# Kernel optimization log

Hardware: AMD Instinct MI355X
Metric: run time of the kernel (lower is better)

The kernel has to match this reference:

```python
import jax, jax.numpy as jnp
import numpy as np

EPS = 1e-5
DIM = 1024

def layer_norm(x, gamma, beta):
    mu = jnp.mean(x, axis=-1, keepdims=True)
    var = jnp.var(x, axis=-1, keepdims=True)
    return (x - mu) * jax.lax.rsqrt(var + EPS) * gamma + beta

def setup_inputs() -> dict:
    key = jax.random.key(0)
    k1, k2 = jax.random.split(key)
    return {
        "image_features": jax.random.normal(k1, (32, 1024, DIM), dtype=jnp.float32),
        "text_features": jax.random.normal(k2, (32, 512, DIM), dtype=jnp.float32),
        "gamma": jnp.ones((DIM,), dtype=jnp.float32),
        "beta": jnp.zeros((DIM,), dtype=jnp.float32),
    }

def reference(image_features, text_features, gamma, beta):
    scale = DIM ** (-0.5)
    image_norm = layer_norm(image_features, gamma, beta)   # [B, Ni, D]
    text_norm = layer_norm(text_features, gamma, beta)     # [B, Nt, D]
    # shared attention matrix, softmax only over text axis
    attn = jax.nn.softmax(jnp.einsum('bid,btd->bit', image_norm, text_norm) * scale, axis=-1)  # [B, Ni, Nt]
    image_attended = jnp.einsum('bit,btd->bid', attn, text_norm)   # [B, Ni, D]
    text_attended = jnp.einsum('bit,bid->btd', attn, image_norm)   # [B, Nt, D] (attn reused transposed, no re-softmax)
    return (image_features + image_attended, text_features + text_attended)
```

## Files before the change

### kernel.cpp

```cpp
#include <hip/hip_runtime.h>
#include <hip/hip_bf16.h>

#define B_  32
#define NI_ 1024
#define NT_ 512
#define D_  1024

typedef __attribute__((ext_vector_type(8))) short bf16x8;
typedef __attribute__((ext_vector_type(4))) float f32x4;

__device__ __forceinline__ ushort f2b(float f) {
  unsigned u = __builtin_bit_cast(unsigned, f);
  u = (u + 0x7FFFu + ((u >> 16) & 1u)) >> 16;
  return (ushort)u;
}


__global__ __launch_bounds__(256) void ln_bf16_kernel(
    const float* __restrict__ x, const float* __restrict__ gamma,
    const float* __restrict__ beta, ushort* __restrict__ out)
{
  const int row  = blockIdx.x * 4 + (threadIdx.x >> 6);
  const int lane = threadIdx.x & 63;
  const float* xr = x + (size_t)row * D_;
  float4 v[4];
  float s = 0.f, sq = 0.f;
#pragma unroll
  for (int q = 0; q < 4; ++q) {
    v[q] = *reinterpret_cast<const float4*>(xr + q * 256 + lane * 4);
    s  += v[q].x + v[q].y + v[q].z + v[q].w;
    sq += v[q].x*v[q].x + v[q].y*v[q].y + v[q].z*v[q].z + v[q].w*v[q].w;
  }
#pragma unroll
  for (int m = 1; m < 64; m <<= 1) {
    s  += __shfl_xor(s,  m);
    sq += __shfl_xor(sq, m);
  }
  const float mean = s * (1.f / D_);
  const float rstd = rsqrtf(sq * (1.f / D_) - mean * mean + 1e-5f);
  ushort* orow = out + (size_t)row * D_;
#pragma unroll
  for (int q = 0; q < 4; ++q) {
    const float4 g  = *reinterpret_cast<const float4*>(gamma + q * 256 + lane * 4);
    const float4 bt = *reinterpret_cast<const float4*>(beta  + q * 256 + lane * 4);
    ushort4 o;
    o.x = f2b((v[q].x - mean) * rstd * g.x + bt.x);
    o.y = f2b((v[q].y - mean) * rstd * g.y + bt.y);
    o.z = f2b((v[q].z - mean) * rstd * g.z + bt.z);
    o.w = f2b((v[q].w - mean) * rstd * g.w + bt.w);
    *reinterpret_cast<ushort4*>(orow + q * 256 + lane * 4) = o;
  }
}

__global__ __launch_bounds__(256) void transpose_bf16_kernel(
    const ushort* __restrict__ in, ushort* __restrict__ out, int R, int C)
{
  __shared__ ushort lds[64][68];
  const size_t nb = (size_t)blockIdx.z * (size_t)R * C;
  const ushort* ib = in + nb;
  ushort* ob = out + nb;
  const int c0 = blockIdx.x * 64, r0 = blockIdx.y * 64;
  const int t = threadIdx.x;
#pragma unroll
  for (int it = 0; it < 2; ++it) {
    const int r = (t >> 3) + 32 * it;
    const int c = (t & 7) * 8;
    uint4 val = *reinterpret_cast<const uint4*>(ib + (size_t)(r0 + r) * C + c0 + c);
    *reinterpret_cast<uint2*>(&lds[r][c])     = make_uint2(val.x, val.y);
    *reinterpret_cast<uint2*>(&lds[r][c + 4]) = make_uint2(val.z, val.w);
  }
  __syncthreads();
#pragma unroll
  for (int it = 0; it < 2; ++it) {
    const int c  = (t >> 3) + 32 * it;
    const int rb = (t & 7) * 8;
    union { ushort u[8]; uint4 v; } pk;
#pragma unroll
    for (int j = 0; j < 8; ++j) pk.u[j] = lds[rb + j][c];
    *reinterpret_cast<uint4*>(ob + (size_t)(c0 + c) * R + r0 + rb) = pk.v;
  }
}

__global__ __launch_bounds__(512) void qk_softmax_kernel(
    const ushort* __restrict__ qn,
    const ushort* __restrict__ kn,
    ushort* __restrict__ attn_it,
    ushort* __restrict__ attn_ti)
{
  __shared__ __align__(16) ushort Asm[2][64 * 32];
  __shared__ __align__(16) ushort Bsm[2][512 * 32];
  __shared__ __align__(16) float redm[64][8];
  __shared__ __align__(16) float reds[64][8];

  const int bid = blockIdx.x;
  const int sid = (bid & 7) * 64 + (bid >> 3);
  const int b   = sid >> 4;
  const int i0  = (sid & 15) * 64;
  const int tid  = threadIdx.x;
  const int w    = tid >> 6;
  const int lane = tid & 63;
  const int lr   = lane & 15;
  const int g    = lane >> 4;

  const ushort* qb = qn + ((size_t)b * NI_ + i0) * D_;
  const ushort* kb = kn + (size_t)b * NT_ * D_;

  const int srow = tid >> 2;
  const int scol = (tid & 3) * 8;
  const int wp = (((tid >> 6) << 6) | (((tid >> 2) & 15) << 2)
                | ((tid & 3) ^ ((tid >> 3) & 3))) * 8;
  const int chunkLane = ((lane & 15) << 2) | ((lane >> 4) ^ ((lane >> 1) & 3));

  uint4 ra, rb0, rb1, rb2, rb3;
  auto LOAD = [&](int t) {
    const int ko = t * 32 + scol;
    if (tid < 256) ra = *reinterpret_cast<const uint4*>(qb + (size_t)srow * D_ + ko);
    rb0 = *reinterpret_cast<const uint4*>(kb + (size_t)(srow      ) * D_ + ko);
    rb1 = *reinterpret_cast<const uint4*>(kb + (size_t)(srow + 128) * D_ + ko);
    rb2 = *reinterpret_cast<const uint4*>(kb + (size_t)(srow + 256) * D_ + ko);
    rb3 = *reinterpret_cast<const uint4*>(kb + (size_t)(srow + 384) * D_ + ko);
  };
  auto WRITE = [&](int nb) {
    if (tid < 256) *reinterpret_cast<uint4*>(&Asm[nb][wp]) = ra;
    *reinterpret_cast<uint4*>(&Bsm[nb][wp        ]) = rb0;
    *reinterpret_cast<uint4*>(&Bsm[nb][wp +  4096]) = rb1;
    *reinterpret_cast<uint4*>(&Bsm[nb][wp +  8192]) = rb2;
    *reinterpret_cast<uint4*>(&Bsm[nb][wp + 12288]) = rb3;
  };

  f32x4 acc[4][4];
#pragma unroll
  for (int i = 0; i < 4; ++i)
#pragma unroll
    for (int j = 0; j < 4; ++j) acc[i][j] = (f32x4){0.f, 0.f, 0.f, 0.f};

  LOAD(0); WRITE(0); __syncthreads();
  const int nst = D_ / 32;
  int cur = 0;
  for (int t = 0; t < nst; ++t) {
    if (t + 1 < nst) LOAD(t + 1);
    const ushort* As = Asm[cur];
    const ushort* Bs = Bsm[cur];
    bf16x8 af[4], bf[4];
#pragma unroll
    for (int i = 0; i < 4; ++i)
      af[i] = *reinterpret_cast<const bf16x8*>(As + (i * 64 + chunkLane) * 8);
#pragma unroll
    for (int j = 0; j < 4; ++j)
      bf[j] = *reinterpret_cast<const bf16x8*>(Bs + ((w * 4 + j) * 64 + chunkLane) * 8);
#pragma unroll
    for (int i = 0; i < 4; ++i)
#pragma unroll
      for (int j = 0; j < 4; ++j)
        acc[i][j] = __builtin_amdgcn_mfma_f32_16x16x32_bf16(af[i], bf[j], acc[i][j], 0, 0, 0);
    __syncthreads();
    if (t + 1 < nst) WRITE(cur ^ 1);
    __syncthreads();
    cur ^= 1;
  }

  const float c1 = 0.03125f * 1.44269504f;

  float mx[4][4];
#pragma unroll
  for (int i = 0; i < 4; ++i)
#pragma unroll
    for (int r = 0; r < 4; ++r) {
      float m = fmaxf(fmaxf(acc[i][0][r], acc[i][1][r]),
                      fmaxf(acc[i][2][r], acc[i][3][r]));
      m = fmaxf(m, __shfl_xor(m, 1));
      m = fmaxf(m, __shfl_xor(m, 2));
      m = fmaxf(m, __shfl_xor(m, 4));
      m = fmaxf(m, __shfl_xor(m, 8));
      mx[i][r] = m;
    }
  if (lr == 0) {
#pragma unroll
    for (int i = 0; i < 4; ++i)
#pragma unroll
      for (int r = 0; r < 4; ++r) redm[i * 16 + g * 4 + r][w] = mx[i][r];
  }
  __syncthreads();
  float gm[4][4];
#pragma unroll
  for (int i = 0; i < 4; ++i)
#pragma unroll
    for (int r = 0; r < 4; ++r) {
      const int row = i * 16 + g * 4 + r;
      const float4 a0 = *reinterpret_cast<const float4*>(&redm[row][0]);
      const float4 a1 = *reinterpret_cast<const float4*>(&redm[row][4]);
      gm[i][r] = fmaxf(fmaxf(fmaxf(a0.x, a0.y), fmaxf(a0.z, a0.w)),
                       fmaxf(fmaxf(a1.x, a1.y), fmaxf(a1.z, a1.w)));
    }

  float sm[4][4];
#pragma unroll
  for (int i = 0; i < 4; ++i)
#pragma unroll
    for (int r = 0; r < 4; ++r) sm[i][r] = 0.f;
#pragma unroll
  for (int i = 0; i < 4; ++i)
#pragma unroll
    for (int j = 0; j < 4; ++j)
#pragma unroll
      for (int r = 0; r < 4; ++r) {
        const float p = exp2f((acc[i][j][r] - gm[i][r]) * c1);
        acc[i][j][r] = p;
        sm[i][r] += p;
      }
#pragma unroll
  for (int i = 0; i < 4; ++i)
#pragma unroll
    for (int r = 0; r < 4; ++r) {
      float s = sm[i][r];
      s += __shfl_xor(s, 1);
      s += __shfl_xor(s, 2);
      s += __shfl_xor(s, 4);
      s += __shfl_xor(s, 8);
      sm[i][r] = s;
    }
  if (lr == 0) {
#pragma unroll
    for (int i = 0; i < 4; ++i)
#pragma unroll
      for (int r = 0; r < 4; ++r) reds[i * 16 + g * 4 + r][w] = sm[i][r];
  }
  __syncthreads();
  float inv[4][4];
#pragma unroll
  for (int i = 0; i < 4; ++i)
#pragma unroll
    for (int r = 0; r < 4; ++r) {
      const int row = i * 16 + g * 4 + r;
      const float4 a0 = *reinterpret_cast<const float4*>(&reds[row][0]);
      const float4 a1 = *reinterpret_cast<const float4*>(&reds[row][4]);
      inv[i][r] = 1.f / (a0.x + a0.y + a0.z + a0.w + a1.x + a1.y + a1.z + a1.w);
    }

#pragma unroll
  for (int i = 0; i < 4; ++i) {
    const int rbase = i0 + i * 16 + g * 4;
#pragma unroll
    for (int j = 0; j < 4; ++j) {
      const int tcol = w * 64 + j * 16 + lr;
      ushort4 pk;
      pk.x = f2b(acc[i][j][0] * inv[i][0]);
      pk.y = f2b(acc[i][j][1] * inv[i][1]);
      pk.z = f2b(acc[i][j][2] * inv[i][2]);
      pk.w = f2b(acc[i][j][3] * inv[i][3]);
      ushort* it_p = attn_it + ((size_t)b * NI_ + rbase) * NT_ + tcol;
      it_p[0 * NT_] = pk.x;
      it_p[1 * NT_] = pk.y;
      it_p[2 * NT_] = pk.z;
      it_p[3 * NT_] = pk.w;
      *reinterpret_cast<ushort4*>(attn_ti + ((size_t)b * NT_ + tcol) * NI_ + rbase) = pk;
    }
  }
}

__global__ __launch_bounds__(256) void bt_gemm_add_kernel(
    const ushort* __restrict__ A,
    const ushort* __restrict__ Bm,
    const float* __restrict__ add,
    float* __restrict__ out,
    int M, int N, int K)
{
  __shared__ __align__(16) ushort Asm[2][128 * 32];
  __shared__ __align__(16) ushort Bsm[2][128 * 32];

  const int b    = blockIdx.z;
  const int m0   = blockIdx.y * 128;
  const int n0   = blockIdx.x * 128;
  const int tid  = threadIdx.x;
  const int w    = tid >> 6;
  const int lane = tid & 63;
  const int lr   = lane & 15;
  const int g    = lane >> 4;

  const ushort* Ab = A  + ((size_t)b * M + m0) * K;
  const ushort* Bb = Bm + ((size_t)b * N + n0) * K;

  const int srow = tid >> 2;
  const int scol = (tid & 3) * 8;
  const int wp = (((tid >> 6) << 6) | (((tid >> 2) & 15) << 2)
                | ((tid & 3) ^ ((tid >> 3) & 3))) * 8;
  const int chunkLane = ((lane & 15) << 2) | ((lane >> 4) ^ ((lane >> 1) & 3));

  uint4 ra0, ra1, rbx0, rbx1;
  auto LOAD = [&](int t) {
    const int ko = t * 32 + scol;
    ra0  = *reinterpret_cast<const uint4*>(Ab + (size_t)(srow     ) * K + ko);
    ra1  = *reinterpret_cast<const uint4*>(Ab + (size_t)(srow + 64) * K + ko);
    rbx0 = *reinterpret_cast<const uint4*>(Bb + (size_t)(srow     ) * K + ko);
    rbx1 = *reinterpret_cast<const uint4*>(Bb + (size_t)(srow + 64) * K + ko);
  };
  auto WRITE = [&](int nb) {
    *reinterpret_cast<uint4*>(&Asm[nb][wp       ]) = ra0;
    *reinterpret_cast<uint4*>(&Asm[nb][wp + 2048]) = ra1;
    *reinterpret_cast<uint4*>(&Bsm[nb][wp       ]) = rbx0;
    *reinterpret_cast<uint4*>(&Bsm[nb][wp + 2048]) = rbx1;
  };

  f32x4 acc[4][4];
#pragma unroll
  for (int i = 0; i < 4; ++i)
#pragma unroll
    for (int j = 0; j < 4; ++j) acc[i][j] = (f32x4){0.f, 0.f, 0.f, 0.f};

  LOAD(0); WRITE(0); __syncthreads();
  const int nst = K / 32;
  int cur = 0;
  for (int t = 0; t < nst; ++t) {
    if (t + 1 < nst) LOAD(t + 1);
    const ushort* As = Asm[cur];
    const ushort* Bs = Bsm[cur];
    bf16x8 af[4], bf[4];
#pragma unroll
    for (int i = 0; i < 4; ++i)
      af[i] = *reinterpret_cast<const bf16x8*>(
          As + (((w >> 1) * 4 + i) * 64 + chunkLane) * 8);
#pragma unroll
    for (int j = 0; j < 4; ++j)
      bf[j] = *reinterpret_cast<const bf16x8*>(
          Bs + (((w & 1) * 4 + j) * 64 + chunkLane) * 8);
#pragma unroll
    for (int i = 0; i < 4; ++i)
#pragma unroll
      for (int j = 0; j < 4; ++j)
        acc[i][j] = __builtin_amdgcn_mfma_f32_16x16x32_bf16(af[i], bf[j], acc[i][j], 0, 0, 0);
    __syncthreads();
    if (t + 1 < nst) WRITE(cur ^ 1);
    __syncthreads();
    cur ^= 1;
  }

  const size_t ob = (size_t)b * M * N;
  const int rbase = m0 + (w >> 1) * 64 + g * 4;
#pragma unroll
  for (int i = 0; i < 4; ++i)
#pragma unroll
    for (int j = 0; j < 4; ++j) {
      const int c = n0 + (w & 1) * 64 + j * 16 + lr;
#pragma unroll
      for (int r = 0; r < 4; ++r) {
        const size_t idx = ob + (size_t)(rbase + i * 16 + r) * N + c;
        out[idx] = add[idx] + acc[i][j][r];
      }
    }
}

extern "C" void kernel_launch(void* const* d_in, const int* in_sizes, int n_in,
                              void* d_out, int out_size, void* d_ws, size_t ws_size,
                              hipStream_t stream) {
  const float* imgf  = (const float*)d_in[0];
  const float* txtf  = (const float*)d_in[1];
  const float* gamma = (const float*)d_in[2];
  const float* beta  = (const float*)d_in[3];

  float* out0 = (float*)d_out;
  float* out1 = out0 + (size_t)B_ * NI_ * D_;

  const size_t SZ = (size_t)B_ * NT_ * NI_ * 2;
  char* ws = (char*)d_ws;
  ushort* attn_ti = (ushort*)ws;
  ushort* attn_it = (ushort*)(ws + SZ);
  ushort* txnT    = (ushort*)(ws + 2 * SZ);
  ushort* imnT    = (ushort*)(ws + SZ);
  ushort* imn     = (ushort*)out1;
  ushort* txn     = (ushort*)out0;

  ln_bf16_kernel<<<(B_ * NI_) / 4, 256, 0, stream>>>(imgf, gamma, beta, imn);
  ln_bf16_kernel<<<(B_ * NT_) / 4, 256, 0, stream>>>(txtf, gamma, beta, txn);
  qk_softmax_kernel<<<(NI_ / 64) * B_, 512, 0, stream>>>(imn, txn, attn_it, attn_ti);
  transpose_bf16_kernel<<<dim3(D_ / 64, NT_ / 64, B_), 256, 0, stream>>>(txn, txnT, NT_, D_);
  bt_gemm_add_kernel<<<dim3(D_ / 128, NI_ / 128, B_), 256, 0, stream>>>(
      attn_it, txnT, imgf, out0, NI_, D_, NT_);
  transpose_bf16_kernel<<<dim3(D_ / 64, NI_ / 64, B_), 256, 0, stream>>>(imn, imnT, NI_, D_);
  bt_gemm_add_kernel<<<dim3(D_ / 128, NT_ / 128, B_), 256, 0, stream>>>(
      attn_ti, imnT, txtf, out1, NT_, D_, NI_);
}
```

Before: 334.5 us.

## Use direct global-to-LDS loads with a four-stage pipeline in the output GEMM

The bt_gemm_add kernel now stages its A and B tiles through global_load_lds, which writes straight into shared memory without passing through registers. The LDS ring grows from two buffers to four and runs three tiles ahead, synchronised with explicit vmcnt waits and a single barrier per k-step instead of two. The aim is to hide global-load latency and drop the register round trip and one barrier. In exchange it uses more LDS, which may lower occupancy. The bank-conflict swizzle is removed in favour of a linear fragment layout, so LDS reads may conflict, and the race-freedom of the four-buffer reuse depends on the barrier ordering.

Result: slower. 364.2 us (+8.9%).

```diff
diff --git a/kernel.cpp b/kernel.cpp
--- a/kernel.cpp
+++ b/kernel.cpp
@@ -15,6 +15,13 @@
   return (ushort)u;
 }
 
+__device__ __forceinline__ void gll16(const ushort* g, ushort* l) {
+  __builtin_amdgcn_global_load_lds(
+      (const __attribute__((address_space(1))) void*)g,
+      (__attribute__((address_space(3))) void*)l, 16, 0, 0);
+}
+
+#define VMWAIT(N) asm volatile("s_waitcnt vmcnt(" #N ")" ::: "memory")
 
 __global__ __launch_bounds__(256) void ln_bf16_kernel(
     const float* __restrict__ x, const float* __restrict__ gamma,
@@ -265,8 +272,8 @@
     float* __restrict__ out,
     int M, int N, int K)
 {
-  __shared__ __align__(16) ushort Asm[2][128 * 32];
-  __shared__ __align__(16) ushort Bsm[2][128 * 32];
+  __shared__ __align__(16) ushort Asm[4][128 * 32];
+  __shared__ __align__(16) ushort Bsm[4][128 * 32];
 
   const int b    = blockIdx.z;
   const int m0   = blockIdx.y * 128;
@@ -280,26 +287,20 @@
   const ushort* Ab = A  + ((size_t)b * M + m0) * K;
   const ushort* Bb = Bm + ((size_t)b * N + n0) * K;
 
-  const int srow = tid >> 2;
-  const int scol = (tid & 3) * 8;
-  const int wp = (((tid >> 6) << 6) | (((tid >> 2) & 15) << 2)
-                | ((tid & 3) ^ ((tid >> 3) & 3))) * 8;
-  const int chunkLane = ((lane & 15) << 2) | ((lane >> 4) ^ ((lane >> 1) & 3));
-
-  uint4 ra0, ra1, rbx0, rbx1;
-  auto LOAD = [&](int t) {
-    const int ko = t * 32 + scol;
-    ra0  = *reinterpret_cast<const uint4*>(Ab + (size_t)(srow     ) * K + ko);
-    ra1  = *reinterpret_cast<const uint4*>(Ab + (size_t)(srow + 64) * K + ko);
-    rbx0 = *reinterpret_cast<const uint4*>(Bb + (size_t)(srow     ) * K + ko);
-    rbx1 = *reinterpret_cast<const uint4*>(Bb + (size_t)(srow + 64) * K + ko);
+  auto ISSUE = [&](int u) {
+    const int nb = u & 3;
+    const int ko = u * 32;
+#pragma unroll
+    for (int q = 0; q < 2; ++q) {
+      const int c   = q * 256 + tid;
+      const int row = ((c >> 6) << 4) | (c & 15);
+      const int kc  = (c >> 4) & 3;
+      const size_t go = (size_t)row * K + ko + kc * 8;
+      const int lbase = (q * 256 + w * 64) * 8;
+      gll16(Ab + go, &Asm[nb][lbase]);
+      gll16(Bb + go, &Bsm[nb][lbase]);
+    }
   };
-  auto WRITE = [&](int nb) {
-    *reinterpret_cast<uint4*>(&Asm[nb][wp       ]) = ra0;
-    *reinterpret_cast<uint4*>(&Asm[nb][wp + 2048]) = ra1;
-    *reinterpret_cast<uint4*>(&Bsm[nb][wp       ]) = rbx0;
-    *reinterpret_cast<uint4*>(&Bsm[nb][wp + 2048]) = rbx1;
-  };
 
   f32x4 acc[4][4];
 #pragma unroll
@@ -307,31 +308,35 @@
 #pragma unroll
     for (int j = 0; j < 4; ++j) acc[i][j] = (f32x4){0.f, 0.f, 0.f, 0.f};
 
-  LOAD(0); WRITE(0); __syncthreads();
   const int nst = K / 32;
-  int cur = 0;
+  ISSUE(0); ISSUE(1); ISSUE(2);
+
   for (int t = 0; t < nst; ++t) {
-    if (t + 1 < nst) LOAD(t + 1);
-    const ushort* As = Asm[cur];
-    const ushort* Bs = Bsm[cur];
+    if (t + 2 < nst)      VMWAIT(8);
+    else if (t + 1 < nst) VMWAIT(4);
+    else                  VMWAIT(0);
+    __builtin_amdgcn_sched_barrier(0);
+    __builtin_amdgcn_s_barrier();
+    __builtin_amdgcn_sched_barrier(0);
+
+    const ushort* As = Asm[t & 3];
+    const ushort* Bs = Bsm[t & 3];
     bf16x8 af[4], bf[4];
 #pragma unroll
     for (int i = 0; i < 4; ++i)
       af[i] = *reinterpret_cast<const bf16x8*>(
-          As + (((w >> 1) * 4 + i) * 64 + chunkLane) * 8);
+          As + (((w >> 1) * 4 + i) * 64 + lane) * 8);
 #pragma unroll
     for (int j = 0; j < 4; ++j)
       bf[j] = *reinterpret_cast<const bf16x8*>(
-          Bs + (((w & 1) * 4 + j) * 64 + chunkLane) * 8);
+          Bs + (((w & 1) * 4 + j) * 64 + lane) * 8);
 #pragma unroll
     for (int i = 0; i < 4; ++i)
 #pragma unroll
       for (int j = 0; j < 4; ++j)
         acc[i][j] = __builtin_amdgcn_mfma_f32_16x16x32_bf16(af[i], bf[j], acc[i][j], 0, 0, 0);
-    __syncthreads();
-    if (t + 1 < nst) WRITE(cur ^ 1);
-    __syncthreads();
-    cur ^= 1;
+
+    if (t + 3 < nst) ISSUE(t + 3);
   }
 
   const size_t ob = (size_t)b * M * N;
```

## Fuse attn·V GEMM and residual add into QK-softmax kernel

Applied to the files above, without the earlier changes.

The QK-softmax kernel now keeps its normalized 64x512 attention tile in shared memory and multiplies it directly by the transposed text features to produce image_attended plus the residual. This drops the separate image-side GEMM launch and the write and re-read of the attn_it matrix. In exchange, the fused kernel loads V operands straight from global memory with no LDS staging or double buffering, holds 128 more accumulator registers per thread, and makes uncoalesced scalar fp32 output stores, which may lower occupancy and efficiency. Workspace buffers are also reassigned so the normalized inputs no longer alias the output tensors.

Result: slower. 363.7 us (+8.7%).

```diff
diff --git a/kernel.cpp b/kernel.cpp
--- a/kernel.cpp
+++ b/kernel.cpp
@@ -14,7 +14,6 @@
   u = (u + 0x7FFFu + ((u >> 16) & 1u)) >> 16;
   return (ushort)u;
 }
-
 
 __global__ __launch_bounds__(256) void ln_bf16_kernel(
     const float* __restrict__ x, const float* __restrict__ gamma,
@@ -81,14 +80,15 @@
   }
 }
 
-__global__ __launch_bounds__(512) void qk_softmax_kernel(
+__global__ __launch_bounds__(512) void attn_fused_kernel(
     const ushort* __restrict__ qn,
     const ushort* __restrict__ kn,
-    ushort* __restrict__ attn_it,
-    ushort* __restrict__ attn_ti)
+    const ushort* __restrict__ vt,
+    const float*  __restrict__ addm,
+    ushort* __restrict__ attn_ti,
+    float*  __restrict__ out0)
 {
-  __shared__ __align__(16) ushort Asm[2][64 * 32];
-  __shared__ __align__(16) ushort Bsm[2][512 * 32];
+  __shared__ __align__(16) ushort raw[36864];
   __shared__ __align__(16) float redm[64][8];
   __shared__ __align__(16) float reds[64][8];
 
@@ -121,11 +121,13 @@
     rb3 = *reinterpret_cast<const uint4*>(kb + (size_t)(srow + 384) * D_ + ko);
   };
   auto WRITE = [&](int nb) {
-    if (tid < 256) *reinterpret_cast<uint4*>(&Asm[nb][wp]) = ra;
-    *reinterpret_cast<uint4*>(&Bsm[nb][wp        ]) = rb0;
-    *reinterpret_cast<uint4*>(&Bsm[nb][wp +  4096]) = rb1;
-    *reinterpret_cast<uint4*>(&Bsm[nb][wp +  8192]) = rb2;
-    *reinterpret_cast<uint4*>(&Bsm[nb][wp + 12288]) = rb3;
+    ushort* As = raw + nb * 2048;
+    ushort* Bs = raw + 4096 + nb * 16384;
+    if (tid < 256) *reinterpret_cast<uint4*>(&As[wp]) = ra;
+    *reinterpret_cast<uint4*>(&Bs[wp        ]) = rb0;
+    *reinterpret_cast<uint4*>(&Bs[wp +  4096]) = rb1;
+    *reinterpret_cast<uint4*>(&Bs[wp +  8192]) = rb2;
+    *reinterpret_cast<uint4*>(&Bs[wp + 12288]) = rb3;
   };
 
   f32x4 acc[4][4];
@@ -139,8 +141,8 @@
   int cur = 0;
   for (int t = 0; t < nst; ++t) {
     if (t + 1 < nst) LOAD(t + 1);
-    const ushort* As = Asm[cur];
-    const ushort* Bs = Bsm[cur];
+    const ushort* As = raw + cur * 2048;
+    const ushort* Bs = raw + 4096 + cur * 16384;
     bf16x8 af[4], bf[4];
 #pragma unroll
     for (int i = 0; i < 4; ++i)
@@ -237,6 +239,7 @@
       inv[i][r] = 1.f / (a0.x + a0.y + a0.z + a0.w + a1.x + a1.y + a1.z + a1.w);
     }
 
+  ushort* P = raw;
 #pragma unroll
   for (int i = 0; i < 4; ++i) {
     const int rbase = i0 + i * 16 + g * 4;
@@ -248,14 +251,53 @@
       pk.y = f2b(acc[i][j][1] * inv[i][1]);
       pk.z = f2b(acc[i][j][2] * inv[i][2]);
       pk.w = f2b(acc[i][j][3] * inv[i][3]);
-      ushort* it_p = attn_it + ((size_t)b * NI_ + rbase) * NT_ + tcol;
-      it_p[0 * NT_] = pk.x;
-      it_p[1 * NT_] = pk.y;
-      it_p[2 * NT_] = pk.z;
-      it_p[3 * NT_] = pk.w;
       *reinterpret_cast<ushort4*>(attn_ti + ((size_t)b * NT_ + tcol) * NI_ + rbase) = pk;
-    }
-  }
+      const int prow = i * 16 + g * 4;
+      P[(prow + 0) * 520 + tcol] = pk.x;
+      P[(prow + 1) * 520 + tcol] = pk.y;
+      P[(prow + 2) * 520 + tcol] = pk.z;
+      P[(prow + 3) * 520 + tcol] = pk.w;
+    }
+  }
+  __syncthreads();
+
+  f32x4 apv[4][8];
+#pragma unroll
+  for (int i = 0; i < 4; ++i)
+#pragma unroll
+    for (int n = 0; n < 8; ++n) apv[i][n] = (f32x4){0.f, 0.f, 0.f, 0.f};
+
+  const ushort* vb = vt + (size_t)b * D_ * NT_;
+#pragma unroll 1
+  for (int ts = 0; ts < NT_ / 32; ++ts) {
+    bf16x8 paf[4], pbf[8];
+#pragma unroll
+    for (int i = 0; i < 4; ++i)
+      paf[i] = *reinterpret_cast<const bf16x8*>(P + (i * 16 + lr) * 520 + ts * 32 + g * 8);
+#pragma unroll
+    for (int n = 0; n < 8; ++n)
+      pbf[n] = *reinterpret_cast<const bf16x8*>(
+          vb + (size_t)(w * 128 + n * 16 + lr) * NT_ + ts * 32 + g * 8);
+#pragma unroll
+    for (int i = 0; i < 4; ++i)
+#pragma unroll
+      for (int n = 0; n < 8; ++n)
+        apv[i][n] = __builtin_amdgcn_mfma_f32_16x16x32_bf16(paf[i], pbf[n], apv[i][n], 0, 0, 0);
+  }
+
+  const float* addb = addm + ((size_t)b * NI_ + i0) * D_;
+  float* outb = out0 + ((size_t)b * NI_ + i0) * D_;
+#pragma unroll
+  for (int i = 0; i < 4; ++i)
+#pragma unroll
+    for (int n = 0; n < 8; ++n) {
+      const int col = w * 128 + n * 16 + lr;
+#pragma unroll
+      for (int r = 0; r < 4; ++r) {
+        const int idx = (i * 16 + g * 4 + r) * D_ + col;
+        outb[idx] = addb[idx] + apv[i][n][r];
+      }
+    }
 }
 
 __global__ __launch_bounds__(256) void bt_gemm_add_kernel(
@@ -360,21 +402,19 @@
   float* out0 = (float*)d_out;
   float* out1 = out0 + (size_t)B_ * NI_ * D_;
 
-  const size_t SZ = (size_t)B_ * NT_ * NI_ * 2;
+  const size_t MB32 = (size_t)B_ * NT_ * NI_ * 2;
   char* ws = (char*)d_ws;
   ushort* attn_ti = (ushort*)ws;
-  ushort* attn_it = (ushort*)(ws + SZ);
-  ushort* txnT    = (ushort*)(ws + 2 * SZ);
-  ushort* imnT    = (ushort*)(ws + SZ);
-  ushort* imn     = (ushort*)out1;
-  ushort* txn     = (ushort*)out0;
+  ushort* txnT    = (ushort*)(ws +     MB32);
+  ushort* imnT    = (ushort*)(ws + 2 * MB32);
+  ushort* txn     = (ushort*)(ws + 4 * MB32);
+  ushort* imn     = (ushort*)(ws + 5 * MB32);
 
   ln_bf16_kernel<<<(B_ * NI_) / 4, 256, 0, stream>>>(imgf, gamma, beta, imn);
   ln_bf16_kernel<<<(B_ * NT_) / 4, 256, 0, stream>>>(txtf, gamma, beta, txn);
-  qk_softmax_kernel<<<(NI_ / 64) * B_, 512, 0, stream>>>(imn, txn, attn_it, attn_ti);
   transpose_bf16_kernel<<<dim3(D_ / 64, NT_ / 64, B_), 256, 0, stream>>>(txn, txnT, NT_, D_);
-  bt_gemm_add_kernel<<<dim3(D_ / 128, NI_ / 128, B_), 256, 0, stream>>>(
-      attn_it, txnT, imgf, out0, NI_, D_, NT_);
+  attn_fused_kernel<<<(NI_ / 64) * B_, 512, 0, stream>>>(
+      imn, txn, txnT, imgf, attn_ti, out0);
   transpose_bf16_kernel<<<dim3(D_ / 64, NI_ / 64, B_), 256, 0, stream>>>(imn, imnT, NI_, D_);
   bt_gemm_add_kernel<<<dim3(D_ / 128, NT_ / 128, B_), 256, 0, stream>>>(
       attn_ti, imnT, txtf, out1, NT_, D_, NI_);
```

## Store attention and transposed operands in MFMA-ready panel layout for GEMMs

Applied to the files above, without the earlier changes.

The softmax and transpose kernels now write their bf16 outputs directly into a tiled panel layout of 128-row by 32-k tiles, already in the MFMA fragment order. The GEMM kernel can then load each tile with fully contiguous 16-byte reads and copy it into LDS without swizzling or scattered strided row access. The cost is more scattered 2-byte and 8-byte stores in the softmax epilogue. Workspace usage also grows, because normalized inputs move from the output buffers into separate workspace regions, and the unswizzled LDS reads may hit bank conflicts.

Measured after the change: 359.2 us. +7.4%, slower.

```diff
diff --git a/kernel.cpp b/kernel.cpp
--- a/kernel.cpp
+++ b/kernel.cpp
@@ -52,15 +52,14 @@
   }
 }
 
-__global__ __launch_bounds__(256) void transpose_bf16_kernel(
-    const ushort* __restrict__ in, ushort* __restrict__ out, int R, int C)
+__global__ __launch_bounds__(256) void transpose_pan_kernel(
+    const ushort* __restrict__ in, ushort* __restrict__ outp, int R, int C)
 {
   __shared__ ushort lds[64][68];
-  const size_t nb = (size_t)blockIdx.z * (size_t)R * C;
-  const ushort* ib = in + nb;
-  ushort* ob = out + nb;
+  const ushort* ib = in + (size_t)blockIdx.z * (size_t)R * C;
   const int c0 = blockIdx.x * 64, r0 = blockIdx.y * 64;
   const int t = threadIdx.x;
+  const int nMT = C >> 7, nKS = R >> 5;
 #pragma unroll
   for (int it = 0; it < 2; ++it) {
     const int r = (t >> 3) + 32 * it;
@@ -77,15 +76,19 @@
     union { ushort u[8]; uint4 v; } pk;
 #pragma unroll
     for (int j = 0; j < 8; ++j) pk.u[j] = lds[rb + j][c];
-    *reinterpret_cast<uint4*>(ob + (size_t)(c0 + c) * R + r0 + rb) = pk.v;
+    const int n  = c0 + c;
+    const int kb = r0 + rb;
+    const size_t tb = ((size_t)blockIdx.z * nMT + (n >> 7)) * nKS + (kb >> 5);
+    const int ch = (((n & 127) >> 4) << 6) | (((kb >> 3) & 3) << 4) | (n & 15);
+    *reinterpret_cast<uint4*>(outp + tb * 4096 + ch * 8) = pk.v;
   }
 }
 
 __global__ __launch_bounds__(512) void qk_softmax_kernel(
     const ushort* __restrict__ qn,
     const ushort* __restrict__ kn,
-    ushort* __restrict__ attn_it,
-    ushort* __restrict__ attn_ti)
+    ushort* __restrict__ ap5,
+    ushort* __restrict__ ap7)
 {
   __shared__ __align__(16) ushort Asm[2][64 * 32];
   __shared__ __align__(16) ushort Bsm[2][512 * 32];
@@ -237,9 +240,14 @@
       inv[i][r] = 1.f / (a0.x + a0.y + a0.z + a0.w + a1.x + a1.y + a1.z + a1.w);
     }
 
+  const int mt5 = i0 >> 7;
 #pragma unroll
   for (int i = 0; i < 4; ++i) {
     const int rbase = i0 + i * 16 + g * 4;
+    const int R5hi  = ((i0 >> 6) & 1) * 4 + i;
+    const int ks7   = rbase >> 5;
+    const int kc7   = (rbase >> 3) & 3;
+    const int el7   = rbase & 7;
 #pragma unroll
     for (int j = 0; j < 4; ++j) {
       const int tcol = w * 64 + j * 16 + lr;
@@ -248,19 +256,23 @@
       pk.y = f2b(acc[i][j][1] * inv[i][1]);
       pk.z = f2b(acc[i][j][2] * inv[i][2]);
       pk.w = f2b(acc[i][j][3] * inv[i][3]);
-      ushort* it_p = attn_it + ((size_t)b * NI_ + rbase) * NT_ + tcol;
-      it_p[0 * NT_] = pk.x;
-      it_p[1 * NT_] = pk.y;
-      it_p[2 * NT_] = pk.z;
-      it_p[3 * NT_] = pk.w;
-      *reinterpret_cast<ushort4*>(attn_ti + ((size_t)b * NT_ + tcol) * NI_ + rbase) = pk;
+      const size_t tb7 = ((size_t)(b * 4 + (tcol >> 7)) * 32 + ks7) * 4096;
+      const int c7 = (((tcol & 127) >> 4) << 6) | (kc7 << 4) | lr;
+      *reinterpret_cast<ushort4*>(ap7 + tb7 + c7 * 8 + el7) = pk;
+      const size_t tb5 = ((size_t)(b * 8 + mt5) * 16 + (tcol >> 5)) * 4096;
+      const int c5 = (R5hi << 6) | (((tcol >> 3) & 3) << 4) | (g * 4);
+      ushort* p5 = ap5 + tb5 + (size_t)c5 * 8 + (tcol & 7);
+      p5[0]  = pk.x;
+      p5[8]  = pk.y;
+      p5[16] = pk.z;
+      p5[24] = pk.w;
     }
   }
 }
 
 __global__ __launch_bounds__(256) void bt_gemm_add_kernel(
-    const ushort* __restrict__ A,
-    const ushort* __restrict__ Bm,
+    const ushort* __restrict__ Apan,
+    const ushort* __restrict__ Bpan,
     const float* __restrict__ add,
     float* __restrict__ out,
     int M, int N, int K)
@@ -276,29 +288,25 @@
   const int lane = tid & 63;
   const int lr   = lane & 15;
   const int g    = lane >> 4;
-
-  const ushort* Ab = A  + ((size_t)b * M + m0) * K;
-  const ushort* Bb = Bm + ((size_t)b * N + n0) * K;
-
-  const int srow = tid >> 2;
-  const int scol = (tid & 3) * 8;
-  const int wp = (((tid >> 6) << 6) | (((tid >> 2) & 15) << 2)
-                | ((tid & 3) ^ ((tid >> 3) & 3))) * 8;
-  const int chunkLane = ((lane & 15) << 2) | ((lane >> 4) ^ ((lane >> 1) & 3));
+  const int nst  = K / 32;
+
+  const ushort* Ab = Apan + ((size_t)(b * (M >> 7) + (m0 >> 7)) * nst) * 4096;
+  const ushort* Bb = Bpan + ((size_t)(b * (N >> 7) + (n0 >> 7)) * nst) * 4096;
 
   uint4 ra0, ra1, rbx0, rbx1;
   auto LOAD = [&](int t) {
-    const int ko = t * 32 + scol;
-    ra0  = *reinterpret_cast<const uint4*>(Ab + (size_t)(srow     ) * K + ko);
-    ra1  = *reinterpret_cast<const uint4*>(Ab + (size_t)(srow + 64) * K + ko);
-    rbx0 = *reinterpret_cast<const uint4*>(Bb + (size_t)(srow     ) * K + ko);
-    rbx1 = *reinterpret_cast<const uint4*>(Bb + (size_t)(srow + 64) * K + ko);
+    const ushort* at = Ab + (size_t)t * 4096;
+    const ushort* bt = Bb + (size_t)t * 4096;
+    ra0  = *reinterpret_cast<const uint4*>(at + tid * 8);
+    ra1  = *reinterpret_cast<const uint4*>(at + 2048 + tid * 8);
+    rbx0 = *reinterpret_cast<const uint4*>(bt + tid * 8);
+    rbx1 = *reinterpret_cast<const uint4*>(bt + 2048 + tid * 8);
   };
   auto WRITE = [&](int nb) {
-    *reinterpret_cast<uint4*>(&Asm[nb][wp       ]) = ra0;
-    *reinterpret_cast<uint4*>(&Asm[nb][wp + 2048]) = ra1;
-    *reinterpret_cast<uint4*>(&Bsm[nb][wp       ]) = rbx0;
-    *reinterpret_cast<uint4*>(&Bsm[nb][wp + 2048]) = rbx1;
+    *reinterpret_cast<uint4*>(&Asm[nb][tid * 8       ]) = ra0;
+    *reinterpret_cast<uint4*>(&Asm[nb][tid * 8 + 2048]) = ra1;
+    *reinterpret_cast<uint4*>(&Bsm[nb][tid * 8       ]) = rbx0;
+    *reinterpret_cast<uint4*>(&Bsm[nb][tid * 8 + 2048]) = rbx1;
   };
 
   f32x4 acc[4][4];
@@ -308,7 +316,6 @@
     for (int j = 0; j < 4; ++j) acc[i][j] = (f32x4){0.f, 0.f, 0.f, 0.f};
 
   LOAD(0); WRITE(0); __syncthreads();
-  const int nst = K / 32;
   int cur = 0;
   for (int t = 0; t < nst; ++t) {
     if (t + 1 < nst) LOAD(t + 1);
@@ -318,11 +325,11 @@
 #pragma unroll
     for (int i = 0; i < 4; ++i)
       af[i] = *reinterpret_cast<const bf16x8*>(
-          As + (((w >> 1) * 4 + i) * 64 + chunkLane) * 8);
+          As + (((w >> 1) * 4 + i) * 64 + lane) * 8);
 #pragma unroll
     for (int j = 0; j < 4; ++j)
       bf[j] = *reinterpret_cast<const bf16x8*>(
-          Bs + (((w & 1) * 4 + j) * 64 + chunkLane) * 8);
+          Bs + (((w & 1) * 4 + j) * 64 + lane) * 8);
 #pragma unroll
     for (int i = 0; i < 4; ++i)
 #pragma unroll
@@ -360,22 +367,22 @@
   float* out0 = (float*)d_out;
   float* out1 = out0 + (size_t)B_ * NI_ * D_;
 
-  const size_t SZ = (size_t)B_ * NT_ * NI_ * 2;
+  const size_t MB32 = (size_t)B_ * NT_ * NI_ * 2;
   char* ws = (char*)d_ws;
-  ushort* attn_ti = (ushort*)ws;
-  ushort* attn_it = (ushort*)(ws + SZ);
-  ushort* txnT    = (ushort*)(ws + 2 * SZ);
-  ushort* imnT    = (ushort*)(ws + SZ);
-  ushort* imn     = (ushort*)out1;
-  ushort* txn     = (ushort*)out0;
+  ushort* ap_it = (ushort*)ws;
+  ushort* ap_ti = (ushort*)(ws +     MB32);
+  ushort* txnT  = (ushort*)(ws + 2 * MB32);
+  ushort* imnT  = (ushort*)(ws + 3 * MB32);
+  ushort* txn   = (ushort*)(ws + 5 * MB32);
+  ushort* imn   = (ushort*)(ws + 6 * MB32);
 
   ln_bf16_kernel<<<(B_ * NI_) / 4, 256, 0, stream>>>(imgf, gamma, beta, imn);
   ln_bf16_kernel<<<(B_ * NT_) / 4, 256, 0, stream>>>(txtf, gamma, beta, txn);
-  qk_softmax_kernel<<<(NI_ / 64) * B_, 512, 0, stream>>>(imn, txn, attn_it, attn_ti);
-  transpose_bf16_kernel<<<dim3(D_ / 64, NT_ / 64, B_), 256, 0, stream>>>(txn, txnT, NT_, D_);
+  qk_softmax_kernel<<<(NI_ / 64) * B_, 512, 0, stream>>>(imn, txn, ap_it, ap_ti);
+  transpose_pan_kernel<<<dim3(D_ / 64, NT_ / 64, B_), 256, 0, stream>>>(txn, txnT, NT_, D_);
   bt_gemm_add_kernel<<<dim3(D_ / 128, NI_ / 128, B_), 256, 0, stream>>>(
-      attn_it, txnT, imgf, out0, NI_, D_, NT_);
-  transpose_bf16_kernel<<<dim3(D_ / 64, NI_ / 64, B_), 256, 0, stream>>>(imn, imnT, NI_, D_);
+      ap_it, txnT, imgf, out0, NI_, D_, NT_);
+  transpose_pan_kernel<<<dim3(D_ / 64, NI_ / 64, B_), 256, 0, stream>>>(imn, imnT, NI_, D_);
   bt_gemm_add_kernel<<<dim3(D_ / 128, NT_ / 128, B_), 256, 0, stream>>>(
-      attn_ti, imnT, txtf, out1, NT_, D_, NI_);
-}
+      ap_ti, imnT, txtf, out1, NT_, D_, NI_);
+}
```
